# Optimization experiments

Hardware: AMD Instinct MI355X
Metric: run time of the kernel (lower is better)

## Reference

```python
import jax, jax.numpy as jnp
import numpy as np

R = 0.4          # ball radius
K = 32           # max_neighbors
S = 512          # cluster_num
BN_EPS = 1e-5


def fps(data, npoint):
    """Furthest point sampling. data: [B,N,C] -> idx [B,npoint] int32.
    Deterministic start at index 0 (original uses randint)."""
    B, N, C = data.shape

    def step(carry, _):
        dist, far = carry
        cent = jnp.take_along_axis(data, far[:, None, None], axis=1)  # [B,1,C]
        d = jnp.sum((data - cent) ** 2, -1)                           # [B,N]
        dist = jnp.minimum(dist, d)
        new_far = jnp.argmax(dist, -1).astype(jnp.int32)
        return (dist, new_far), far

    dist0 = jnp.full((B, N), 1e10, data.dtype)
    far0 = jnp.zeros((B,), jnp.int32)
    _, idxs = jax.lax.scan(step, (dist0, far0), None, length=npoint)
    return idxs.T  # [B,npoint]


def gather_points(data, idx):
    """data [B,N,C], idx [B,S] -> [B,S,C]"""
    return jnp.take_along_axis(data, idx[..., None], axis=1)


def gather_groups(data, idx):
    """data [B,N,C], idx [B,S,K] -> [B,S,K,C]"""
    B, N, C = data.shape
    _, Sq, Kq = idx.shape
    flat = jnp.take_along_axis(data, idx.reshape(B, Sq * Kq)[..., None], axis=1)
    return flat.reshape(B, Sq, Kq, C)


def square_dist(a, b):
    """a [B,N,C], b [B,M,C] -> [B,N,M]"""
    return (-2.0 * jnp.einsum('bnc,bmc->bnm', a, b)
            + jnp.sum(a ** 2, -1)[:, :, None]
            + jnp.sum(b ** 2, -1)[:, None, :])


def knn_query(data, query, max_neighbors, r):
    """Ball query: indices of up to max_neighbors points within r, padded with
    the first valid index. data [B,N,C], query [B,S,C] -> [B,S,K] int32."""
    B, N, _ = data.shape
    d = square_dist(query, data)                              # [B,S,N]
    idx = jnp.where(d <= r * r, jnp.arange(N, dtype=jnp.int32)[None, None, :], N)
    idx = jnp.sort(idx, axis=-1)[:, :, :max_neighbors]        # ascending, N = invalid
    first = idx[:, :, :1]
    return jnp.where(idx == N, first, idx)


def mlp_layer(x, w, b, g, be):
    """1x1 Conv2d + BatchNorm2d (training-mode batch stats) + ReLU.
    x [B,S,K,Cin], w [Cout,Cin] -> [B,S,K,Cout]"""
    y = jnp.einsum('bskc,oc->bsko', x, w) + b
    m = jnp.mean(y, axis=(0, 1, 2))
    v = jnp.var(y, axis=(0, 1, 2))
    y = (y - m) * jax.lax.rsqrt(v + BN_EPS) * g + be
    return jax.nn.relu(y)


def setup_inputs() -> dict:
    key = jax.random.key(0)
    ks = jax.random.split(key, 5)
    B, N = 16, 8192
    data = jax.random.normal(ks[0], (B, N, 3), jnp.float32)
    data_feature = jax.random.normal(ks[1], (B, N, 3), jnp.float32)
    w0 = jax.random.normal(ks[2], (64, 6), jnp.float32) * 0.1
    w1 = jax.random.normal(ks[3], (64, 64), jnp.float32) * 0.1
    w2 = jax.random.normal(ks[4], (128, 64), jnp.float32) * 0.1
    zeros = lambda c: jnp.zeros((c,), jnp.float32)
    ones = lambda c: jnp.ones((c,), jnp.float32)
    return dict(data=data, data_feature=data_feature,
                w0=w0, b0=zeros(64), g0=ones(64), be0=zeros(64),
                w1=w1, b1=zeros(64), g1=ones(64), be1=zeros(64),
                w2=w2, b2=zeros(128), g2=ones(128), be2=zeros(128))


def reference(data, data_feature, w0, b0, g0, be0, w1, b1, g1, be1, w2, b2, g2, be2):
    B, N, C = data.shape
    fps_idx = fps(data, S)                              # [B,S]
    centroids = gather_points(data, fps_idx)            # [B,S,3]
    nbr_idx = knn_query(data, centroids, K, R)          # [B,S,K]
    sample = gather_groups(data, nbr_idx)               # [B,S,K,3]
    sample_norm = sample - centroids[:, :, None, :]
    feat = gather_groups(data_feature, nbr_idx)         # [B,S,K,3]
    x = jnp.concatenate([sample_norm, feat], axis=-1)   # [B,S,K,6]
    x = mlp_layer(x, w0, b0, g0, be0)
    x = mlp_layer(x, w1, b1, g1, be1)
    x = mlp_layer(x, w2, b2, g2, be2)
    out = jnp.max(x, axis=2)                            # [B,S,128]
    return centroids, out
```

## Files before the change

### kernel.cpp

```cpp
#include <hip/hip_runtime.h>
#include <math.h>

constexpr int Bc = 16;
constexpr int Nc = 8192;
constexpr int Sc = 512;
constexpr int Kc = 32;
constexpr int Pc = Bc * Sc * Kc;

template <int CTRL>
__device__ __forceinline__ float dpp_max_stage(float x) {
  int p = __builtin_amdgcn_update_dpp(0, __float_as_int(x), CTRL, 0xf, 0xf, true);
  return fmaxf(x, __int_as_float(p));
}

__global__ __launch_bounds__(256, 1)
void fps_kernel(const float* __restrict__ data,
                float* __restrict__ cent_out,
                float* __restrict__ cent_ws) {
  const int b = blockIdx.x;
  const int t = threadIdx.x;
  const int lane = t & 63, w = t >> 6;

  __shared__ float lx[Nc], ly[Nc], lz[Nc];
  __shared__ unsigned long long red_k[2][4];
  __shared__ int idx_hist[Sc];

  const float* db = data + (size_t)b * Nc * 3;

  float px[32], py[32], pz[32], dist[32];
#pragma unroll
  for (int j = 0; j < 32; ++j) {
    int p = t + 256 * j;
    px[j] = db[p * 3 + 0];
    py[j] = db[p * 3 + 1];
    pz[j] = db[p * 3 + 2];
    dist[j] = 1e10f;
    lx[p] = px[j]; ly[p] = py[j]; lz[p] = pz[j];
  }
  __syncthreads();

  int far = 0;
  for (int it = 0; it < Sc; ++it) {
    const int sfar = __builtin_amdgcn_readfirstlane(far);
    if (t == 0) idx_hist[it] = sfar;
    const float cx = lx[sfar];
    const float cy = ly[sfar];
    const float cz = lz[sfar];

    float best = -1.0f; int bj = 0;
#pragma unroll
    for (int j = 0; j < 32; ++j) {
      float dx = __fsub_rn(px[j], cx);
      float dy = __fsub_rn(py[j], cy);
      float dz = __fsub_rn(pz[j], cz);
      float d = __fadd_rn(__fadd_rn(__fmul_rn(dx, dx), __fmul_rn(dy, dy)),
                          __fmul_rn(dz, dz));
      float nd = fminf(dist[j], d);
      dist[j] = nd;
      if (nd > best) { best = nd; bj = j; }
    }
    const int bidx = t + 256 * bj;

    float wmax = best;
    wmax = dpp_max_stage<0xB1>(wmax);
    wmax = dpp_max_stage<0x4E>(wmax);
    wmax = dpp_max_stage<0x141>(wmax);
    wmax = dpp_max_stage<0x140>(wmax);
    wmax = fmaxf(wmax, __shfl_xor(wmax, 16));
    wmax = fmaxf(wmax, __shfl_xor(wmax, 32));

    unsigned long long m = __ballot(best == wmax);
    int idx;
    if (__popcll(m) == 1) {
      idx = __shfl(bidx, (int)__ffsll((long long)m) - 1);
    } else {
      int cand = (best == wmax) ? bidx : 0x7fffffff;
#pragma unroll
      for (int off = 32; off; off >>= 1) cand = min(cand, __shfl_xor(cand, off));
      idx = cand;
    }

    unsigned long long key =
        ((unsigned long long)__float_as_uint(wmax) << 32) |
        (unsigned long long)(0xFFFFFFFFu - (unsigned)idx);
    const int par = it & 1;
    if (lane == 0) red_k[par][w] = key;
    __syncthreads();

    unsigned long long k0 = red_k[par][0];
    unsigned long long k1 = red_k[par][1];
    unsigned long long k2 = red_k[par][2];
    unsigned long long k3 = red_k[par][3];
    unsigned long long ka = (k0 > k1) ? k0 : k1;
    unsigned long long kb = (k2 > k3) ? k2 : k3;
    unsigned long long kk = (ka > kb) ? ka : kb;
    far = (int)(0xFFFFFFFFu - (unsigned)(kk & 0xFFFFFFFFull));
  }

  __syncthreads();
  for (int s = t; s < Sc; s += 256) {
    int id = idx_hist[s];
    float vx = lx[id], vy = ly[id], vz = lz[id];
    size_t o = ((size_t)b * Sc + s) * 3;
    cent_out[o + 0] = vx; cent_out[o + 1] = vy; cent_out[o + 2] = vz;
    cent_ws[o + 0]  = vx; cent_ws[o + 1]  = vy; cent_ws[o + 2]  = vz;
  }
}

__global__ __launch_bounds__(256)
void ball_kernel(const float* __restrict__ data,
                 const float* __restrict__ feat,
                 const float* __restrict__ cent_ws,
                 float* __restrict__ x0) {
  const int w = threadIdx.x >> 6, lane = threadIdx.x & 63;
  const int q = blockIdx.x * 4 + w;
  const int b = q >> 9;
  const float* db = data + (size_t)b * Nc * 3;
  const float* fb = feat + (size_t)b * Nc * 3;

  const float qx = cent_ws[q * 3 + 0];
  const float qy = cent_ws[q * 3 + 1];
  const float qz = cent_ws[q * 3 + 2];
  const float q2 = __fadd_rn(__fadd_rn(__fmul_rn(qx, qx), __fmul_rn(qy, qy)),
                             __fmul_rn(qz, qz));

  __shared__ int nbr[4][Kc];
  int have = 0;
  for (int base = 0; base < Nc; base += 64) {
    int i = base + lane;
    float px = db[i * 3 + 0], py = db[i * 3 + 1], pz = db[i * 3 + 2];
    float p2 = __fadd_rn(__fadd_rn(__fmul_rn(px, px), __fmul_rn(py, py)),
                         __fmul_rn(pz, pz));
    float dt = fmaf(qz, pz, fmaf(qy, py, __fmul_rn(qx, px)));
    float d = __fadd_rn(__fadd_rn(__fmul_rn(-2.0f, dt), q2), p2);
    bool ok = d <= 0.16f;
    unsigned long long mask = __ballot(ok);
    if (mask) {
      int pos = have + __popcll(mask & ((1ull << lane) - 1ull));
      if (ok && pos < Kc) nbr[w][pos] = i;
      have += __popcll(mask);
      if (have >= Kc) break;
    }
  }
  if (have > Kc) have = Kc;
  __syncthreads();

  if (lane < Kc) {
    int k = lane;
    int j = nbr[w][k < have ? k : 0];
    float sx = __fsub_rn(db[j * 3 + 0], qx);
    float sy = __fsub_rn(db[j * 3 + 1], qy);
    float sz = __fsub_rn(db[j * 3 + 2], qz);
    float fx = fb[j * 3 + 0], fy = fb[j * 3 + 1], fz = fb[j * 3 + 2];
    size_t pidx = (size_t)q * Kc + k;
    x0[(size_t)0 * Pc + pidx] = sx;
    x0[(size_t)1 * Pc + pidx] = sy;
    x0[(size_t)2 * Pc + pidx] = sz;
    x0[(size_t)3 * Pc + pidx] = fx;
    x0[(size_t)4 * Pc + pidx] = fy;
    x0[(size_t)5 * Pc + pidx] = fz;
  }
}

__global__ __launch_bounds__(256)
void pass_a(const float* __restrict__ x0, const float* __restrict__ w0,
            const float* __restrict__ b0, float* __restrict__ part0) {
  const int lane = threadIdx.x & 63, w = threadIdx.x >> 6;
  const int slice = blockIdx.x * 4 + w;
  const int o = lane;
  float W[6];
#pragma unroll
  for (int c = 0; c < 6; ++c) W[c] = w0[o * 6 + c];
  const float bias = b0[o];
  float sum = 0.f, sq = 0.f;
  const int pps = Pc / 4096;
  const int p0 = slice * pps;
  for (int j = 0; j < pps; ++j) {
    int p = p0 + j;
    float y = bias;
#pragma unroll
    for (int c = 0; c < 6; ++c) y = fmaf(x0[(size_t)c * Pc + p], W[c], y);
    sum += y;
    sq = fmaf(y, y, sq);
  }
  __shared__ float bsum[64], bsq[64];
  if (threadIdx.x < 64) { bsum[threadIdx.x] = 0.f; bsq[threadIdx.x] = 0.f; }
  __syncthreads();
  atomicAdd(&bsum[o], sum);
  atomicAdd(&bsq[o], sq);
  __syncthreads();
  if (threadIdx.x < 64)       part0[blockIdx.x * 128 + threadIdx.x] = bsum[threadIdx.x];
  else if (threadIdx.x < 128) part0[blockIdx.x * 128 + threadIdx.x] = bsq[threadIdx.x - 64];
}

__global__ __launch_bounds__(256)
void reduce_k(const float* __restrict__ part, int nblk, int nch,
              const float* __restrict__ g, const float* __restrict__ be,
              float* __restrict__ AB) {
  const int o = blockIdx.x;
  const int t = threadIdx.x;
  double sum = 0.0, sq = 0.0;
  for (int i = t; i < nblk; i += 256) {
    sum += (double)part[(size_t)i * (2 * nch) + o];
    sq  += (double)part[(size_t)i * (2 * nch) + nch + o];
  }
  __shared__ double ls[256], lq[256];
  ls[t] = sum; lq[t] = sq;
  __syncthreads();
  for (int s = 128; s > 0; s >>= 1) {
    if (t < s) { ls[t] += ls[t + s]; lq[t] += lq[t + s]; }
    __syncthreads();
  }
  if (t == 0) {
    double m = ls[0] / (double)Pc;
    double v = lq[0] / (double)Pc - m * m;
    double A = (double)g[o] / sqrt(v + 1e-5);
    AB[o] = (float)A;
    AB[nch + o] = (float)((double)be[o] - m * A);
  }
}

__global__ __launch_bounds__(256)
void pass_b(const float* __restrict__ x0, const float* __restrict__ w0,
            const float* __restrict__ b0, const float* __restrict__ AB0,
            const float* __restrict__ w1, const float* __restrict__ b1,
            float* __restrict__ y1, float* __restrict__ part1) {
  const int p = blockIdx.x * 256 + threadIdx.x;
  const int lane = threadIdx.x & 63, w = threadIdx.x >> 6;

  float xin[6];
#pragma unroll
  for (int c = 0; c < 6; ++c) xin[c] = x0[(size_t)c * Pc + p];

  float x1[64];
#pragma unroll
  for (int o = 0; o < 64; ++o) {
    float y = b0[o];
#pragma unroll
    for (int c = 0; c < 6; ++c) y = fmaf(xin[c], w0[o * 6 + c], y);
    x1[o] = fmaxf(fmaf(y, AB0[o], AB0[64 + o]), 0.f);
  }

  __shared__ float ssum[4][64][17], ssq[4][64][17];

  for (int o = 0; o < 64; ++o) {
    float a0 = b1[o], a1 = 0.f, a2 = 0.f, a3 = 0.f;
#pragma unroll
    for (int c = 0; c < 64; c += 4) {
      a0 = fmaf(x1[c + 0], w1[o * 64 + c + 0], a0);
      a1 = fmaf(x1[c + 1], w1[o * 64 + c + 1], a1);
      a2 = fmaf(x1[c + 2], w1[o * 64 + c + 2], a2);
      a3 = fmaf(x1[c + 3], w1[o * 64 + c + 3], a3);
    }
    float acc = (a0 + a1) + (a2 + a3);
    y1[(size_t)o * Pc + p] = acc;

    float sv = acc + __shfl_xor(acc, 1);
    sv += __shfl_xor(sv, 2);
    float q = acc * acc;
    float qv = q + __shfl_xor(q, 1);
    qv += __shfl_xor(qv, 2);
    if ((lane & 3) == 0) {
      ssum[w][o][lane >> 2] = sv;
      ssq[w][o][lane >> 2] = qv;
    }
  }
  __syncthreads();
  if (threadIdx.x < 128) {
    const int o = threadIdx.x & 63;
    const bool isq = threadIdx.x >= 64;
    float s = 0.f;
#pragma unroll
    for (int ww = 0; ww < 4; ++ww)
      for (int k = 0; k < 16; ++k)
        s += isq ? ssq[ww][o][k] : ssum[ww][o][k];
    part1[blockIdx.x * 128 + threadIdx.x] = s;
  }
}

__global__ __launch_bounds__(256)
void pass_c(const float* __restrict__ y1, const float* __restrict__ AB1,
            const float* __restrict__ w2, const float* __restrict__ b2,
            float* __restrict__ maxy2, float* __restrict__ part2) {
  const int p = blockIdx.x * 256 + threadIdx.x;
  const int lane = threadIdx.x & 63, w = threadIdx.x >> 6;
  const int grp = p >> 5;

  float x2[64];
#pragma unroll
  for (int c = 0; c < 64; ++c) {
    float v = y1[(size_t)c * Pc + p];
    x2[c] = fmaxf(fmaf(v, AB1[c], AB1[64 + c]), 0.f);
  }

  __shared__ float ssum[4][128][9], ssq[4][128][9];

  for (int o = 0; o < 128; ++o) {
    float a0 = b2[o], a1 = 0.f, a2 = 0.f, a3 = 0.f;
#pragma unroll
    for (int c = 0; c < 64; c += 4) {
      a0 = fmaf(x2[c + 0], w2[o * 64 + c + 0], a0);
      a1 = fmaf(x2[c + 1], w2[o * 64 + c + 1], a1);
      a2 = fmaf(x2[c + 2], w2[o * 64 + c + 2], a2);
      a3 = fmaf(x2[c + 3], w2[o * 64 + c + 3], a3);
    }
    float acc = (a0 + a1) + (a2 + a3);

    float mx = acc;
#pragma unroll
    for (int off = 16; off > 0; off >>= 1) mx = fmaxf(mx, __shfl_xor(mx, off));
    if ((lane & 31) == 0) maxy2[(size_t)grp * 128 + o] = mx;

    float sv = acc + __shfl_xor(acc, 1);
    sv += __shfl_xor(sv, 2);
    sv += __shfl_xor(sv, 4);
    float q = acc * acc;
    float qv = q + __shfl_xor(q, 1);
    qv += __shfl_xor(qv, 2);
    qv += __shfl_xor(qv, 4);
    if ((lane & 7) == 0) {
      ssum[w][o][lane >> 3] = sv;
      ssq[w][o][lane >> 3] = qv;
    }
  }
  __syncthreads();
  {
    const int o = threadIdx.x & 127;
    const bool isq = threadIdx.x >= 128;
    float s = 0.f;
#pragma unroll
    for (int ww = 0; ww < 4; ++ww)
      for (int k = 0; k < 8; ++k)
        s += isq ? ssq[ww][o][k] : ssum[ww][o][k];
    part2[blockIdx.x * 256 + threadIdx.x] = s;
  }
}

__global__ __launch_bounds__(256)
void final_k(const float* __restrict__ maxy2, const float* __restrict__ AB2,
             float* __restrict__ out) {
  int i = blockIdx.x * 256 + threadIdx.x;
  int o = i & 127;
  out[i] = fmaxf(fmaf(maxy2[i], AB2[o], AB2[128 + o]), 0.f);
}

extern "C" void kernel_launch(void* const* d_in, const int* in_sizes, int n_in,
                              void* d_out, int out_size, void* d_ws, size_t ws_size,
                              hipStream_t stream) {
  const float* data = (const float*)d_in[0];
  const float* feat = (const float*)d_in[1];
  const float* w0 = (const float*)d_in[2];
  const float* b0 = (const float*)d_in[3];
  const float* g0 = (const float*)d_in[4];
  const float* be0 = (const float*)d_in[5];
  const float* w1 = (const float*)d_in[6];
  const float* b1 = (const float*)d_in[7];
  const float* g1 = (const float*)d_in[8];
  const float* be1 = (const float*)d_in[9];
  const float* w2 = (const float*)d_in[10];
  const float* b2 = (const float*)d_in[11];
  const float* g2 = (const float*)d_in[12];
  const float* be2 = (const float*)d_in[13];
  float* out = (float*)d_out;

  float* ws = (float*)d_ws;
  float* cent_ws = ws; ws += (size_t)Bc * Sc * 3;
  float* x0 = ws;      ws += (size_t)6 * Pc;
  float* y1 = ws;      ws += (size_t)64 * Pc;
  float* maxy2 = ws;   ws += (size_t)Bc * Sc * 128;
  float* part0 = ws;   ws += 1024 * 128;
  float* part1 = ws;   ws += 1024 * 128;
  float* part2 = ws;   ws += 1024 * 256;
  float* AB0 = ws;     ws += 128;
  float* AB1 = ws;     ws += 128;
  float* AB2 = ws;     ws += 256;

  fps_kernel<<<Bc, 256, 0, stream>>>(data, out, cent_ws);
  ball_kernel<<<(Bc * Sc) / 4, 256, 0, stream>>>(data, feat, cent_ws, x0);
  pass_a<<<1024, 256, 0, stream>>>(x0, w0, b0, part0);
  reduce_k<<<64, 256, 0, stream>>>(part0, 1024, 64, g0, be0, AB0);
  pass_b<<<Pc / 256, 256, 0, stream>>>(x0, w0, b0, AB0, w1, b1, y1, part1);
  reduce_k<<<64, 256, 0, stream>>>(part1, 1024, 64, g1, be1, AB1);
  pass_c<<<Pc / 256, 256, 0, stream>>>(y1, AB1, w2, b2, maxy2, part2);
  reduce_k<<<128, 256, 0, stream>>>(part2, 1024, 128, g2, be2, AB2);
  final_k<<<(Bc * Sc * 128) / 256, 256, 0, stream>>>(maxy2, AB2, out + (size_t)Bc * Sc * 3);
}
```

Baseline: 812.9 us.

## Fuse layer-0 BN statistics into ball query and BN2 apply into final reduce

After: 816.8 us. No clear change (+0.5%).

```diff
diff --git a/kernel.cpp b/kernel.cpp
--- a/kernel.cpp
+++ b/kernel.cpp
@@ -111,8 +111,12 @@
 void ball_kernel(const float* __restrict__ data,
                  const float* __restrict__ feat,
                  const float* __restrict__ cent_ws,
-                 float* __restrict__ x0) {
+                 const float* __restrict__ w0,
+                 const float* __restrict__ b0,
+                 float* __restrict__ x0,
+                 float* __restrict__ part0) {
   const int w = threadIdx.x >> 6, lane = threadIdx.x & 63;
+  const int t = threadIdx.x;
   const int q = blockIdx.x * 4 + w;
   const int b = q >> 9;
   const float* db = data + (size_t)b * Nc * 3;
@@ -125,6 +129,7 @@
                              __fmul_rn(qz, qz));
 
   __shared__ int nbr[4][Kc];
+  __shared__ float x0s[6][128];
   int have = 0;
   for (int base = 0; base < Nc; base += 64) {
     int i = base + lane;
@@ -159,38 +164,38 @@
     x0[(size_t)3 * Pc + pidx] = fx;
     x0[(size_t)4 * Pc + pidx] = fy;
     x0[(size_t)5 * Pc + pidx] = fz;
-  }
-}
-
-__global__ __launch_bounds__(256)
-void pass_a(const float* __restrict__ x0, const float* __restrict__ w0,
-            const float* __restrict__ b0, float* __restrict__ part0) {
-  const int lane = threadIdx.x & 63, w = threadIdx.x >> 6;
-  const int slice = blockIdx.x * 4 + w;
-  const int o = lane;
+    int col = w * Kc + k;
+    x0s[0][col] = sx; x0s[1][col] = sy; x0s[2][col] = sz;
+    x0s[3][col] = fx; x0s[4][col] = fy; x0s[5][col] = fz;
+  }
+  __syncthreads();
+
+  const int o = t & 63, q4 = t >> 6;
   float W[6];
 #pragma unroll
   for (int c = 0; c < 6; ++c) W[c] = w0[o * 6 + c];
   const float bias = b0[o];
   float sum = 0.f, sq = 0.f;
-  const int pps = Pc / 4096;
-  const int p0 = slice * pps;
-  for (int j = 0; j < pps; ++j) {
-    int p = p0 + j;
+#pragma unroll 4
+  for (int k = 0; k < 32; ++k) {
+    int p = q4 * 32 + k;
     float y = bias;
 #pragma unroll
-    for (int c = 0; c < 6; ++c) y = fmaf(x0[(size_t)c * Pc + p], W[c], y);
+    for (int c = 0; c < 6; ++c) y = fmaf(x0s[c][p], W[c], y);
     sum += y;
     sq = fmaf(y, y, sq);
   }
-  __shared__ float bsum[64], bsq[64];
-  if (threadIdx.x < 64) { bsum[threadIdx.x] = 0.f; bsq[threadIdx.x] = 0.f; }
-  __syncthreads();
-  atomicAdd(&bsum[o], sum);
-  atomicAdd(&bsq[o], sq);
-  __syncthreads();
-  if (threadIdx.x < 64)       part0[blockIdx.x * 128 + threadIdx.x] = bsum[threadIdx.x];
-  else if (threadIdx.x < 128) part0[blockIdx.x * 128 + threadIdx.x] = bsq[threadIdx.x - 64];
+  __shared__ float bsum[4][64], bsq[4][64];
+  bsum[q4][o] = sum; bsq[q4][o] = sq;
+  __syncthreads();
+  if (t < 64)
+    part0[blockIdx.x * 128 + t] =
+        ((bsum[0][t] + bsum[1][t]) + bsum[2][t]) + bsum[3][t];
+  else if (t < 128) {
+    int oo = t - 64;
+    part0[blockIdx.x * 128 + t] =
+        ((bsq[0][oo] + bsq[1][oo]) + bsq[2][oo]) + bsq[3][oo];
+  }
 }
 
 __global__ __launch_bounds__(256)
@@ -221,6 +226,41 @@
 }
 
 __global__ __launch_bounds__(256)
+void reduce2_final_k(const float* __restrict__ part, int nblk,
+                     const float* __restrict__ g, const float* __restrict__ be,
+                     const float* __restrict__ maxy2,
+                     float* __restrict__ out) {
+  const int o = blockIdx.x;
+  const int t = threadIdx.x;
+  double sum = 0.0, sq = 0.0;
+  for (int i = t; i < nblk; i += 256) {
+    sum += (double)part[(size_t)i * 256 + o];
+    sq  += (double)part[(size_t)i * 256 + 128 + o];
+  }
+  __shared__ double ls[256], lq[256];
+  ls[t] = sum; lq[t] = sq;
+  __syncthreads();
+  for (int s = 128; s > 0; s >>= 1) {
+    if (t < s) { ls[t] += ls[t + s]; lq[t] += lq[t + s]; }
+    __syncthreads();
+  }
+  __shared__ float sA, sB;
+  if (t == 0) {
+    double m = ls[0] / (double)Pc;
+    double v = lq[0] / (double)Pc - m * m;
+    double A = (double)g[o] / sqrt(v + 1e-5);
+    sA = (float)A;
+    sB = (float)((double)be[o] - m * A);
+  }
+  __syncthreads();
+  const float A = sA, B = sB;
+  for (int grp = t; grp < Bc * Sc; grp += 256) {
+    float v = maxy2[(size_t)grp * 128 + o];
+    out[(size_t)grp * 128 + o] = fmaxf(fmaf(v, A, B), 0.f);
+  }
+}
+
+__global__ __launch_bounds__(256)
 void pass_b(const float* __restrict__ x0, const float* __restrict__ w0,
             const float* __restrict__ b0, const float* __restrict__ AB0,
             const float* __restrict__ w1, const float* __restrict__ b1,
@@ -334,14 +374,6 @@
         s += isq ? ssq[ww][o][k] : ssum[ww][o][k];
     part2[blockIdx.x * 256 + threadIdx.x] = s;
   }
-}
-
-__global__ __launch_bounds__(256)
-void final_k(const float* __restrict__ maxy2, const float* __restrict__ AB2,
-             float* __restrict__ out) {
-  int i = blockIdx.x * 256 + threadIdx.x;
-  int o = i & 127;
-  out[i] = fmaxf(fmaf(maxy2[i], AB2[o], AB2[128 + o]), 0.f);
 }
 
 extern "C" void kernel_launch(void* const* d_in, const int* in_sizes, int n_in,
@@ -368,20 +400,19 @@
   float* x0 = ws;      ws += (size_t)6 * Pc;
   float* y1 = ws;      ws += (size_t)64 * Pc;
   float* maxy2 = ws;   ws += (size_t)Bc * Sc * 128;
-  float* part0 = ws;   ws += 1024 * 128;
+  float* part0 = ws;   ws += 2048 * 128;
   float* part1 = ws;   ws += 1024 * 128;
   float* part2 = ws;   ws += 1024 * 256;
   float* AB0 = ws;     ws += 128;
   float* AB1 = ws;     ws += 128;
-  float* AB2 = ws;     ws += 256;
 
   fps_kernel<<<Bc, 256, 0, stream>>>(data, out, cent_ws);
-  ball_kernel<<<(Bc * Sc) / 4, 256, 0, stream>>>(data, feat, cent_ws, x0);
-  pass_a<<<1024, 256, 0, stream>>>(x0, w0, b0, part0);
-  reduce_k<<<64, 256, 0, stream>>>(part0, 1024, 64, g0, be0, AB0);
+  ball_kernel<<<(Bc * Sc) / 4, 256, 0, stream>>>(data, feat, cent_ws,
+                                                 w0, b0, x0, part0);
+  reduce_k<<<64, 256, 0, stream>>>(part0, 2048, 64, g0, be0, AB0);
   pass_b<<<Pc / 256, 256, 0, stream>>>(x0, w0, b0, AB0, w1, b1, y1, part1);
   reduce_k<<<64, 256, 0, stream>>>(part1, 1024, 64, g1, be1, AB1);
   pass_c<<<Pc / 256, 256, 0, stream>>>(y1, AB1, w2, b2, maxy2, part2);
-  reduce_k<<<128, 256, 0, stream>>>(part2, 1024, 128, g2, be2, AB2);
-  final_k<<<(Bc * Sc * 128) / 256, 256, 0, stream>>>(maxy2, AB2, out + (size_t)Bc * Sc * 3);
-}
+  reduce2_final_k<<<128, 256, 0, stream>>>(part2, 1024, g2, be2, maxy2,
+                                           out + (size_t)Bc * Sc * 3);
+}
```
